# Kernel optimization log

Measured on AMD Instinct MI355X. Metric: run time of the kernel, lower is better.

## Reference

```python
import jax, jax.numpy as jnp
import numpy as np

M_GROUP = 8  # VENOM m: pattern period along in_features

def _nm_mask(in_features, dtype):
    # NMVectorSparsifier.get_random_mask keeps positions 0 and 2 of every group of m=8
    pat = jnp.array([1.0, 0.0, 1.0, 0.0, 0.0, 0.0, 0.0, 0.0], dtype=dtype)
    return jnp.tile(pat, in_features // M_GROUP)  # [in_features]


def setup_inputs() -> dict:
    key = jax.random.key(0)
    k1, k2, k3 = jax.random.split(key, 3)
    B, S, D_IN, D_OUT = 8, 2048, 4096, 4096
    x = jax.random.normal(k1, (B, S, D_IN), dtype=jnp.float32)
    weight = jax.random.normal(k2, (D_OUT, D_IN), dtype=jnp.float32) * 0.02
    bias = jax.random.normal(k3, (D_OUT,), dtype=jnp.float32) * 0.02
    return {"x": x, "weight": weight, "bias": bias}


def reference(x, weight, bias):
    # y = x @ (W * mask)^T + b  -- N:M (2:8) vector-sparse linear, dense-math reference
    mask = _nm_mask(weight.shape[1], weight.dtype)  # [D_IN]
    w = weight * mask[None, :]                      # [D_OUT, D_IN]
    return jnp.einsum('bsd,od->bso', x, w) + bias
```

## Files before the change

kernel.cpp:

```cpp
#include <hip/hip_runtime.h>
#include <hip/hip_bf16.h>
#include <stdint.h>

#define MROWS 16384
#define DIN   4096
#define DOUT  4096
#define KEFF  1024

typedef __attribute__((ext_vector_type(8))) __bf16 bf16x8;
typedef __attribute__((ext_vector_type(4))) float f32x4;

#define AS1 __attribute__((address_space(1)))
#define AS3 __attribute__((address_space(3)))

__device__ __forceinline__ uint32_t f2bf_rne(float f) {
  union { float f; uint32_t u; } v; v.f = f;
  uint32_t u = v.u;
  return (u + 0x7fffu + ((u >> 16) & 1u)) >> 16;
}

__global__ void venom_gather(const float* __restrict__ src,
                             uint32_t* __restrict__ dst, int ngroups) {
  int stride = gridDim.x * blockDim.x;
  for (int i = blockIdx.x * blockDim.x + threadIdx.x; i < ngroups; i += stride) {
    const float4 v = *reinterpret_cast<const float4*>(src + (size_t)i * 8);
    dst[i] = f2bf_rne(v.x) | (f2bf_rne(v.z) << 16);
  }
}

#define BM 256
#define BN 256
#define BK 64
#define NT (KEFF / BK)

__device__ __forceinline__ int swz_off(int R, int lg) {
  int sr = R >> 1;
  return sr * 128 + (((((R & 1) << 2) | lg) ^ (sr & 7)) << 4);
}

__global__ __launch_bounds__(512, 2) void venom_gemm(
    const __bf16* __restrict__ A, const __bf16* __restrict__ Bm,
    const float* __restrict__ bias, float* __restrict__ C) {
  __shared__ __bf16 As[2][2][128 * 64];
  __shared__ __bf16 Bs[2][2][128 * 64];

  const int nblkN = DOUT / BN;
  int nwg = gridDim.x;
  int cpx = nwg >> 3;
  int bid = blockIdx.x;
  int swz = (bid & 7) * cpx + (bid >> 3);
  int mblk = swz / nblkN;
  int nblk = swz % nblkN;

  int t = threadIdx.x;
  int wid = t >> 6, l = t & 63;
  int wr = wid >> 2, wc = wid & 3;
  int lr = l & 15, lg = l >> 4;

  const __bf16* Ag = A + (size_t)(mblk * BM) * KEFF;
  const __bf16* Bg = Bm + (size_t)(nblk * BN) * KEFF;

  f32x4 acc[8][4] = {};

  auto stage_half = [&](int buf, int kt, int kh) {
    const int k0 = kt * BK + kh * 32;
    #pragma unroll
    for (int i = 0; i < 2; ++i) {
      int e = i * 512 + t;
      int sr = e >> 3;
      int s = (e & 7) ^ (sr & 7);
      int row = sr * 2 + (s >> 2);
      int koff = (s & 3) * 8;
      __builtin_amdgcn_global_load_lds(
          (const AS1 uint32_t*)(Ag + (size_t)row * KEFF + k0 + koff),
          ((AS3 uint32_t*)&As[buf][kh][0]) + e * 4, 16, 0, 0);
      __builtin_amdgcn_global_load_lds(
          (const AS1 uint32_t*)(Bg + (size_t)row * KEFF + k0 + koff),
          ((AS3 uint32_t*)&Bs[buf][kh][0]) + e * 4, 16, 0, 0);
    }
  };

  stage_half(0, 0, 0);
  stage_half(0, 0, 1);
  asm volatile("s_waitcnt vmcnt(4)" ::: "memory");
  __builtin_amdgcn_s_barrier();

  bf16x8 bfrag[4];

  for (int kt = 0; kt < NT; ++kt) {
    const int cur = kt & 1, nxt = cur ^ 1, t1 = kt + 1;

    #pragma unroll
    for (int ph = 0; ph < 4; ++ph) {
      const int mh = ph & 1, kh = ph >> 1;
      const char* aB = (const char*)&As[cur][kh][0];
      bf16x8 af[4];
      #pragma unroll
      for (int mi = 0; mi < 4; ++mi)
        af[mi] = *(const bf16x8*)(aB + swz_off(wr * 128 + mh * 64 + mi * 16 + lr, lg));
      if (mh == 0) {
        const char* bB = (const char*)&Bs[cur][kh][0];
        #pragma unroll
        for (int ni = 0; ni < 4; ++ni)
          bfrag[ni] = *(const bf16x8*)(bB + swz_off(wc * 64 + ni * 16 + lr, lg));
        if (t1 < NT) stage_half(nxt, t1, kh);
      }

      __builtin_amdgcn_s_barrier();
      __builtin_amdgcn_s_setprio(1);
      #pragma unroll
      for (int mi = 0; mi < 4; ++mi)
        #pragma unroll
        for (int ni = 0; ni < 4; ++ni)
          acc[mh * 4 + mi][ni] = __builtin_amdgcn_mfma_f32_16x16x32_bf16(
              af[mi], bfrag[ni], acc[mh * 4 + mi][ni], 0, 0, 0);
      __builtin_amdgcn_s_setprio(0);

      if (ph == 1) {
        if (t1 < NT) asm volatile("s_waitcnt vmcnt(4)" ::: "memory");
        else         asm volatile("s_waitcnt vmcnt(0)" ::: "memory");
        __builtin_amdgcn_s_barrier();
      } else if (ph == 3) {
        if (t1 < NT) {
          asm volatile("s_waitcnt vmcnt(4)" ::: "memory");
          __builtin_amdgcn_s_barrier();
        }
      } else {
        __builtin_amdgcn_s_barrier();
      }
    }
  }

  int colbase = nblk * BN + wc * 64;
  int rowbase = mblk * BM + wr * 128;
  #pragma unroll
  for (int mh = 0; mh < 2; ++mh)
    #pragma unroll
    for (int mi = 0; mi < 4; ++mi) {
      int row0 = rowbase + mh * 64 + mi * 16 + lg * 4;
      #pragma unroll
      for (int ni = 0; ni < 4; ++ni) {
        int col = colbase + ni * 16 + lr;
        float bv = bias[col];
        f32x4 cv = acc[mh * 4 + mi][ni];
        #pragma unroll
        for (int j = 0; j < 4; ++j)
          C[(size_t)(row0 + j) * DOUT + col] = cv[j] + bv;
      }
    }
}

__global__ void venom_naive(const float* __restrict__ x, const float* __restrict__ w,
                            const float* __restrict__ bias, float* __restrict__ out) {
  size_t total = (size_t)MROWS * DOUT;
  size_t stride = (size_t)gridDim.x * blockDim.x;
  for (size_t idx = (size_t)blockIdx.x * blockDim.x + threadIdx.x; idx < total;
       idx += stride) {
    int m = (int)(idx / DOUT), n = (int)(idx % DOUT);
    const float* xr = x + (size_t)m * DIN;
    const float* wr = w + (size_t)n * DIN;
    float s = 0.f;
    for (int g = 0; g < DIN / 8; ++g)
      s += xr[g * 8] * wr[g * 8] + xr[g * 8 + 2] * wr[g * 8 + 2];
    out[idx] = s + bias[n];
  }
}

extern "C" void kernel_launch(void* const* d_in, const int* in_sizes, int n_in,
                              void* d_out, int out_size, void* d_ws, size_t ws_size,
                              hipStream_t stream) {
  const float* x    = (const float*)d_in[0];
  const float* wgt  = (const float*)d_in[1];
  const float* bias = (const float*)d_in[2];
  float* out = (float*)d_out;

  const size_t xg_bytes = (size_t)MROWS * KEFF * 2;
  const size_t wg_bytes = (size_t)DOUT * KEFF * 2;

  if (ws_size < xg_bytes + wg_bytes) {
    venom_naive<<<2048, 256, 0, stream>>>(x, wgt, bias, out);
    return;
  }

  uint32_t* xg = (uint32_t*)d_ws;
  uint32_t* wg = (uint32_t*)((char*)d_ws + xg_bytes);

  venom_gather<<<2048, 256, 0, stream>>>(x, xg, MROWS * (DIN / 8));
  venom_gather<<<512, 256, 0, stream>>>(wgt, wg, DOUT * (DIN / 8));

  venom_gemm<<<(MROWS / BM) * (DOUT / BN), 512, 0, stream>>>(
      (const __bf16*)xg, (const __bf16*)wg, bias, out);
}
```

Baseline: 301.2 us.

## Make GEMM blocks loop over four N tiles with cross-tile prefetch

Each workgroup now handles four consecutive 256-wide N tiles for one M block. The grid shrinks by four, and the next tile's first K slice is prefetched during the previous tile's last iteration, so the pipeline does not drain between tiles. Bias values are preloaded into registers and accumulators are reset after each tile's epilogue. The gather kernel now has each thread process two 8-element groups and write a uint2, and the weight gather uses more blocks. Risks: fewer workgroups (256) may underfill the CUs, and the A tile is reloaded for each N tile anyway.

Measured after the change: 281.8 us. 1.07x faster.

```diff
diff --git a/kernel.cpp b/kernel.cpp
--- a/kernel.cpp
+++ b/kernel.cpp
@@ -19,12 +19,17 @@
   return (u + 0x7fffu + ((u >> 16) & 1u)) >> 16;
 }
 
-__global__ void venom_gather(const float* __restrict__ src,
-                             uint32_t* __restrict__ dst, int ngroups) {
+__global__ void venom_gather2(const float* __restrict__ src,
+                              uint2* __restrict__ dst, int npairs) {
   int stride = gridDim.x * blockDim.x;
-  for (int i = blockIdx.x * blockDim.x + threadIdx.x; i < ngroups; i += stride) {
-    const float4 v = *reinterpret_cast<const float4*>(src + (size_t)i * 8);
-    dst[i] = f2bf_rne(v.x) | (f2bf_rne(v.z) << 16);
+  for (int i = blockIdx.x * blockDim.x + threadIdx.x; i < npairs; i += stride) {
+    const float4* p = reinterpret_cast<const float4*>(src) + (size_t)i * 4;
+    float4 a = p[0];
+    float4 b = p[2];
+    uint2 r;
+    r.x = f2bf_rne(a.x) | (f2bf_rne(a.z) << 16);
+    r.y = f2bf_rne(b.x) | (f2bf_rne(b.z) << 16);
+    dst[i] = r;
   }
 }
 
@@ -32,6 +37,7 @@
 #define BN 256
 #define BK 64
 #define NT (KEFF / BK)
+#define TPB 4
 
 __device__ __forceinline__ int swz_off(int R, int lg) {
   int sr = R >> 1;
@@ -44,13 +50,12 @@
   __shared__ __bf16 As[2][2][128 * 64];
   __shared__ __bf16 Bs[2][2][128 * 64];
 
-  const int nblkN = DOUT / BN;
   int nwg = gridDim.x;
   int cpx = nwg >> 3;
   int bid = blockIdx.x;
   int swz = (bid & 7) * cpx + (bid >> 3);
-  int mblk = swz / nblkN;
-  int nblk = swz % nblkN;
+  int mblk = swz >> 2;
+  int ngrp = swz & 3;
 
   int t = threadIdx.x;
   int wid = t >> 6, l = t & 63;
@@ -58,12 +63,20 @@
   int lr = l & 15, lg = l >> 4;
 
   const __bf16* Ag = A + (size_t)(mblk * BM) * KEFF;
-  const __bf16* Bg = Bm + (size_t)(nblk * BN) * KEFF;
+
+  float biasr[TPB][4];
+  #pragma unroll
+  for (int j = 0; j < TPB; ++j)
+    #pragma unroll
+    for (int ni = 0; ni < 4; ++ni)
+      biasr[j][ni] = bias[(ngrp * TPB + j) * BN + wc * 64 + ni * 16 + lr];
 
   f32x4 acc[8][4] = {};
 
-  auto stage_half = [&](int buf, int kt, int kh) {
-    const int k0 = kt * BK + kh * 32;
+  auto stage_half = [&](int j2, int kt2, int kh) {
+    const int buf = kt2 & 1;
+    const __bf16* Bg = Bm + (size_t)((ngrp * TPB + j2) * BN) * KEFF;
+    const int k0 = kt2 * BK + kh * 32;
     #pragma unroll
     for (int i = 0; i < 2; ++i) {
       int e = i * 512 + t;
@@ -87,67 +100,80 @@
 
   bf16x8 bfrag[4];
 
-  for (int kt = 0; kt < NT; ++kt) {
-    const int cur = kt & 1, nxt = cur ^ 1, t1 = kt + 1;
-
-    #pragma unroll
-    for (int ph = 0; ph < 4; ++ph) {
-      const int mh = ph & 1, kh = ph >> 1;
-      const char* aB = (const char*)&As[cur][kh][0];
-      bf16x8 af[4];
+  #pragma unroll
+  for (int j = 0; j < TPB; ++j) {
+    #pragma unroll 1
+    for (int kt = 0; kt < NT; ++kt) {
+      const int cur = kt & 1;
+      const bool last_it = (j == TPB - 1) && (kt == NT - 1);
+      const int j2  = (kt < NT - 1) ? j : j + 1;
+      const int kt2 = (kt < NT - 1) ? kt + 1 : 0;
+
       #pragma unroll
-      for (int mi = 0; mi < 4; ++mi)
-        af[mi] = *(const bf16x8*)(aB + swz_off(wr * 128 + mh * 64 + mi * 16 + lr, lg));
-      if (mh == 0) {
-        const char* bB = (const char*)&Bs[cur][kh][0];
-        #pragma unroll
-        for (int ni = 0; ni < 4; ++ni)
-          bfrag[ni] = *(const bf16x8*)(bB + swz_off(wc * 64 + ni * 16 + lr, lg));
-        if (t1 < NT) stage_half(nxt, t1, kh);
-      }
-
-      __builtin_amdgcn_s_barrier();
-      __builtin_amdgcn_s_setprio(1);
-      #pragma unroll
-      for (int mi = 0; mi < 4; ++mi)
-        #pragma unroll
-        for (int ni = 0; ni < 4; ++ni)
-          acc[mh * 4 + mi][ni] = __builtin_amdgcn_mfma_f32_16x16x32_bf16(
-              af[mi], bfrag[ni], acc[mh * 4 + mi][ni], 0, 0, 0);
-      __builtin_amdgcn_s_setprio(0);
-
-      if (ph == 1) {
-        if (t1 < NT) asm volatile("s_waitcnt vmcnt(4)" ::: "memory");
-        else         asm volatile("s_waitcnt vmcnt(0)" ::: "memory");
+      for (int ph = 0; ph < 4; ++ph) {
+        const int mh = ph & 1, kh = ph >> 1;
+        const char* aB = (const char*)&As[cur][kh][0];
+        bf16x8 af[4];
+        #pragma unroll
+        for (int mi = 0; mi < 4; ++mi)
+          af[mi] = *(const bf16x8*)(aB + swz_off(wr * 128 + mh * 64 + mi * 16 + lr, lg));
+        if (mh == 0) {
+          const char* bB = (const char*)&Bs[cur][kh][0];
+          #pragma unroll
+          for (int ni = 0; ni < 4; ++ni)
+            bfrag[ni] = *(const bf16x8*)(bB + swz_off(wc * 64 + ni * 16 + lr, lg));
+          if (!last_it) stage_half(j2, kt2, kh);
+        }
+
         __builtin_amdgcn_s_barrier();
-      } else if (ph == 3) {
-        if (t1 < NT) {
-          asm volatile("s_waitcnt vmcnt(4)" ::: "memory");
+        __builtin_amdgcn_s_setprio(1);
+        #pragma unroll
+        for (int mi = 0; mi < 4; ++mi)
+          #pragma unroll
+          for (int ni = 0; ni < 4; ++ni)
+            acc[mh * 4 + mi][ni] = __builtin_amdgcn_mfma_f32_16x16x32_bf16(
+                af[mi], bfrag[ni], acc[mh * 4 + mi][ni], 0, 0, 0);
+        __builtin_amdgcn_s_setprio(0);
+
+        if (ph == 1) {
+          if (!last_it) asm volatile("s_waitcnt vmcnt(4)" ::: "memory");
+          else          asm volatile("s_waitcnt vmcnt(0)" ::: "memory");
+          __builtin_amdgcn_s_barrier();
+        } else if (ph == 3) {
+          if (!last_it) {
+            asm volatile("s_waitcnt vmcnt(4)" ::: "memory");
+            __builtin_amdgcn_s_barrier();
+          }
+        } else {
           __builtin_amdgcn_s_barrier();
         }
-      } else {
-        __builtin_amdgcn_s_barrier();
       }
     }
-  }
-
-  int colbase = nblk * BN + wc * 64;
-  int rowbase = mblk * BM + wr * 128;
-  #pragma unroll
-  for (int mh = 0; mh < 2; ++mh)
-    #pragma unroll
-    for (int mi = 0; mi < 4; ++mi) {
-      int row0 = rowbase + mh * 64 + mi * 16 + lg * 4;
+
+    {
+      int colbase = (ngrp * TPB + j) * BN + wc * 64;
+      int rowbase = mblk * BM + wr * 128;
       #pragma unroll
-      for (int ni = 0; ni < 4; ++ni) {
-        int col = colbase + ni * 16 + lr;
-        float bv = bias[col];
-        f32x4 cv = acc[mh * 4 + mi][ni];
-        #pragma unroll
-        for (int j = 0; j < 4; ++j)
-          C[(size_t)(row0 + j) * DOUT + col] = cv[j] + bv;
-      }
+      for (int mh = 0; mh < 2; ++mh)
+        #pragma unroll
+        for (int mi = 0; mi < 4; ++mi) {
+          int row0 = rowbase + mh * 64 + mi * 16 + lg * 4;
+          #pragma unroll
+          for (int ni = 0; ni < 4; ++ni) {
+            int col = colbase + ni * 16 + lr;
+            f32x4 cv = acc[mh * 4 + mi][ni];
+            #pragma unroll
+            for (int jj = 0; jj < 4; ++jj)
+              C[(size_t)(row0 + jj) * DOUT + col] = cv[jj] + biasr[j][ni];
+          }
+        }
+      #pragma unroll
+      for (int q = 0; q < 8; ++q)
+        #pragma unroll
+        for (int ni = 0; ni < 4; ++ni)
+          acc[q][ni] = (f32x4){0.f, 0.f, 0.f, 0.f};
     }
+  }
 }
 
 __global__ void venom_naive(const float* __restrict__ x, const float* __restrict__ w,
@@ -185,9 +211,9 @@
   uint32_t* xg = (uint32_t*)d_ws;
   uint32_t* wg = (uint32_t*)((char*)d_ws + xg_bytes);
 
-  venom_gather<<<2048, 256, 0, stream>>>(x, xg, MROWS * (DIN / 8));
-  venom_gather<<<512, 256, 0, stream>>>(wgt, wg, DOUT * (DIN / 8));
-
-  venom_gemm<<<(MROWS / BM) * (DOUT / BN), 512, 0, stream>>>(
+  venom_gather2<<<2048, 256, 0, stream>>>(x, (uint2*)xg, MROWS * (DIN / 16));
+  venom_gather2<<<1024, 256, 0, stream>>>(wgt, (uint2*)wg, DOUT * (DIN / 16));
+
+  venom_gemm<<<(MROWS / BM) * (DOUT / BN / TPB), 512, 0, stream>>>(
       (const __bf16*)xg, (const __bf16*)wg, bias, out);
 }
```
